# Kernel optimization log

Hardware: AMD Instinct MI355X
Metric: run time of the kernel (lower is better)

Reference implementation:

```python
import jax, jax.numpy as jnp
import numpy as np

B, T, V, H, L = 2048, 128, 256, 20, 15  # batch, seq_len, vocab, hidden, max_label


def setup_inputs() -> dict:
    key = jax.random.key(0)
    ks = jax.random.split(key, 8)
    g = lambda k, shape, s: (jax.random.normal(k, shape, jnp.float32) * s)
    return {
        "x": jax.random.randint(ks[0], (B, T), 0, V, dtype=jnp.int32),
        "W0": g(ks[1], (V, 3 * H), 0.06),   # input kernel layer 0 [V, 3H] (z|r|h)
        "U0": g(ks[2], (H, 3 * H), 0.2),    # recurrent kernel layer 0
        "b0i": jnp.zeros((3 * H,), jnp.float32),  # input bias (reset_after=True split bias)
        "b0r": jnp.zeros((3 * H,), jnp.float32),  # recurrent bias
        "W1": g(ks[3], (H, 3 * H), 0.2),
        "U1": g(ks[4], (H, 3 * H), 0.2),
        "b1i": jnp.zeros((3 * H,), jnp.float32),
        "b1r": jnp.zeros((3 * H,), jnp.float32),
        "Wd": g(ks[5], (H, L), 0.2),
        "bd": jnp.zeros((L,), jnp.float32),
        "drop_rate": 0,  # identity dropout (deterministic reference)
    }


def _gru_cell(h, xw, U, br):
    # Keras GRUCell with reset_after=True:
    #   xw = x @ W + b_in  (precomputed), rec = h @ U + b_rec
    rec = h @ U + br
    xz, xr, xh = jnp.split(xw, 3, axis=-1)
    rz, rr, rh = jnp.split(rec, 3, axis=-1)
    z = jax.nn.sigmoid(xz + rz)
    r = jax.nn.sigmoid(xr + rr)
    hh = jnp.tanh(xh + r * rh)
    return z * h + (1.0 - z) * hh


def reference(x, W0, U0, b0i, b0r, W1, U1, b1i, b1r, Wd, bd, drop_rate):
    # one_hot(x) @ W0 == gather rows of W0 (same math, no [B,T,V] materialization)
    xW0 = W0[x] + b0i                 # [B, T, 3H]
    xW0 = jnp.swapaxes(xW0, 0, 1)     # [T, B, 3H] for scan over time

    def step(carry, xw_t):
        h0, h1 = carry
        h0 = _gru_cell(h0, xw_t, U0, b0r)
        xw1 = h0 @ W1 + b1i
        h1 = _gru_cell(h1, xw1, U1, b1r)
        return (h0, h1), None

    h0 = jnp.zeros((x.shape[0], H), W0.dtype)
    h1 = jnp.zeros((x.shape[0], H), W0.dtype)
    (h0, h1), _ = jax.lax.scan(step, (h0, h1), xW0)
    # tf.nn.dropout with rate 0 is the identity
    out = h1
    logits = jax.nn.softmax(out @ Wd + bd, axis=-1)  # [B, L]
    return logits
```

## Files before the change

kernel.cpp:

```cpp
#include <hip/hip_runtime.h>


#define BB 2048
#define TT 128
#define HH 20
#define LL 15
#define H3 60

typedef float v2f __attribute__((ext_vector_type(2)));

__device__ __forceinline__ float bclane(float v, int k) {
    return __int_as_float(__builtin_amdgcn_readlane(__float_as_int(v), k));
}
__device__ __forceinline__ float dpp_rshr1(float v) {
    return __int_as_float(__builtin_amdgcn_update_dpp(
        0, __float_as_int(v), 0x111, 0xF, 0xF, true));
}
__device__ __forceinline__ float fast_rcp(float x) { return __builtin_amdgcn_rcpf(x); }
__device__ __forceinline__ float sigm(float x) { return fast_rcp(1.f + __expf(-x)); }
__device__ __forceinline__ float tanh_f(float x) { return 1.f - 2.f * fast_rcp(1.f + __expf(2.f * x)); }
#define PIN(v) asm volatile("" : "+v"(v))
#define LDSFENCE() asm volatile("" ::: "memory")

extern "C" __global__ __launch_bounds__(256)
__attribute__((amdgpu_waves_per_eu(2, 2)))
void gru2_kernel(const int* __restrict__ x, const float* __restrict__ W0,
                 const float* __restrict__ U0, const float* __restrict__ b0i,
                 const float* __restrict__ b0r, const float* __restrict__ W1,
                 const float* __restrict__ U1, const float* __restrict__ b1i,
                 const float* __restrict__ b1r, const float* __restrict__ Wd,
                 const float* __restrict__ bd, float* __restrict__ out)
{
    if (((blockIdx.x >> 3) ^ (blockIdx.x >> 8)) & 1)
        __builtin_amdgcn_s_sleep(6);

    const int lane = threadIdx.x & 63;
    const int w = threadIdx.x >> 6;
    const int b = blockIdx.x * 4 + w;
    const int row = lane >> 4;
    const int pos = lane & 15;
    const int pc  = (pos < 15) ? pos : 14;
    const int u   = pc / 3;
    const int p3  = pc % 3;
    const int j   = row * 5 + u;
    const bool home = (pos < 15) && (p3 == 2);
    const int col = p3 * 20 + j;

    __shared__ __align__(16) float hbuf[4][2][24];
    float* h0buf = &hbuf[w][0][0];
    float* h1buf = &hbuf[w][1][0];
    const float4* h0q = (const float4*)h0buf;
    const float4* h1q = (const float4*)h1buf;
    if (home) { h0buf[j] = 0.f; h1buf[j] = 0.f; }
    LDSFENCE();

    v2f u0p[10], w1p[10], u1p[10];
#pragma unroll
    for (int q = 0; q < 10; ++q) {
        const int k0 = (2 * q) * H3, k1 = (2 * q + 1) * H3;
        u0p[q] = v2f{U0[k0 + col], U0[k1 + col]};
        w1p[q] = v2f{W1[k0 + col], W1[k1 + col]};
        u1p[q] = v2f{U1[k0 + col], U1[k1 + col]};
    }
#pragma unroll
    for (int q = 0; q < 10; ++q) { PIN(u0p[q]); PIN(w1p[q]); PIN(u1p[q]); }
    float bi0 = b0i[col], br0 = b0r[col], bi1 = b1i[col], br1 = b1r[col];
    PIN(bi0); PIN(br0); PIN(bi1); PIN(br1);

    const int* xrow = x + b * TT;
    const int tokA = xrow[lane];
    const int tokB = xrow[64 + lane];

    float h0 = 0.f, h1 = 0.f;

    const int tok0 = __builtin_amdgcn_readlane(tokA, 0);
    const int tok1 = __builtin_amdgcn_readlane(tokA, 1);
    int tokn2 = __builtin_amdgcn_readlane(tokA, 2);
    float xw_cur = W0[tok0 * H3 + col] + bi0;
    float xw_nxt = W0[tok1 * H3 + col];

    float4 c0[5], c1[5];
    float rec0, xw1, rec1;

#define DOTS()                                                                \
    {                                                                         \
        v2f a0a = v2f{br0, 0.f}, a0b = v2f{0.f, 0.f};                         \
        v2f a1a = v2f{bi1, 0.f}, a1b = v2f{0.f, 0.f};                         \
        v2f a2a = v2f{br1, 0.f}, a2b = v2f{0.f, 0.f};                         \
        _Pragma("unroll")                                                     \
        for (int q = 0; q < 5; ++q) {                                         \
            const v2f hA = v2f{c0[q].x, c0[q].y}, hB = v2f{c0[q].z, c0[q].w}; \
            a0a = __builtin_elementwise_fma(hA, u0p[2 * q], a0a);             \
            a0b = __builtin_elementwise_fma(hB, u0p[2 * q + 1], a0b);         \
            a1a = __builtin_elementwise_fma(hA, w1p[2 * q], a1a);             \
            a1b = __builtin_elementwise_fma(hB, w1p[2 * q + 1], a1b);         \
        }                                                                     \
        _Pragma("unroll")                                                     \
        for (int q = 0; q < 5; ++q) {                                         \
            const v2f gA = v2f{c1[q].x, c1[q].y}, gB = v2f{c1[q].z, c1[q].w}; \
            a2a = __builtin_elementwise_fma(gA, u1p[2 * q], a2a);             \
            a2b = __builtin_elementwise_fma(gB, u1p[2 * q + 1], a2b);         \
        }                                                                     \
        { const v2f t = a0a + a0b; rec0 = t.x + t.y; }                        \
        { const v2f t = a1a + a1b; xw1  = t.x + t.y; }                        \
        { const v2f t = a2a + a2b; rec1 = t.x + t.y; }                        \
    }

    {
        const float pf = W0[tokn2 * H3 + col];
        const int tokn3 = __builtin_amdgcn_readlane(tokA, 3);
        const float sg0 = sigm(xw_cur + br0);
        const float rv0 = dpp_rshr1(sg0);
        const float zv0 = dpp_rshr1(rv0);
        const float hh0 = tanh_f(xw_cur + rv0 * br0);
        h0 = fmaf(zv0, h0 - hh0, hh0);
        if (home) h0buf[j] = h0;
        LDSFENCE();
#pragma unroll
        for (int q = 0; q < 5; ++q) { c0[q] = h0q[q]; c1[q] = h1q[q]; }
        xw_cur = xw_nxt + bi0; xw_nxt = pf; tokn2 = tokn3;
        DOTS();
    }

#pragma unroll 2
    for (int i = 1; i < TT; ++i) {
        const int t3 = (i + 3 < TT) ? (i + 3) : (TT - 1);
        const float pf = W0[tokn2 * H3 + col];
        const int tokn3 = __builtin_amdgcn_readlane(t3 < 64 ? tokA : tokB, t3 & 63);

        const float sg0 = sigm(xw_cur + rec0);
        const float rv0 = dpp_rshr1(sg0);
        const float zv0 = dpp_rshr1(rv0);
        const float hh0 = tanh_f(xw_cur + rv0 * rec0);
        h0 = fmaf(zv0, h0 - hh0, hh0);
        if (home) h0buf[j] = h0;
        LDSFENCE();
#pragma unroll
        for (int q = 0; q < 5; ++q) c0[q] = h0q[q];

        const float sg1 = sigm(xw1 + rec1);
        const float rv1 = dpp_rshr1(sg1);
        const float zv1 = dpp_rshr1(rv1);
        const float hh1 = tanh_f(xw1 + rv1 * rec1);
        h1 = fmaf(zv1, h1 - hh1, hh1);
        if (home) h1buf[j] = h1;
        LDSFENCE();
#pragma unroll
        for (int q = 0; q < 5; ++q) c1[q] = h1q[q];

        xw_cur = xw_nxt + bi0; xw_nxt = pf; tokn2 = tokn3;

        DOTS();
    }

    {
        const float sg1 = sigm(xw1 + rec1);
        const float rv1 = dpp_rshr1(sg1);
        const float zv1 = dpp_rshr1(rv1);
        const float hh1 = tanh_f(xw1 + rv1 * rec1);
        h1 = fmaf(zv1, h1 - hh1, hh1);
        if (home) h1buf[j] = h1;
        LDSFENCE();
    }

    const int l = lane < LL ? lane : LL - 1;
    float acc = bd[l];
#pragma unroll
    for (int k = 0; k < HH; ++k)
        acc = fmaf(h1buf[k], Wd[k * LL + l], acc);

    float m = acc;
#pragma unroll
    for (int i = 0; i < LL; ++i) m = fmaxf(m, bclane(acc, i));
    const float e = __expf(acc - m);
    float s = 0.f;
#pragma unroll
    for (int i = 0; i < LL; ++i) s += bclane(e, i);
    const float pr = e * fast_rcp(s);

    if (lane < LL) out[b * LL + lane] = pr;
}

extern "C" void kernel_launch(void* const* d_in, const int* in_sizes, int n_in,
                              void* d_out, int out_size, void* d_ws, size_t ws_size,
                              hipStream_t stream) {
    const int*   x   = (const int*)  d_in[0];
    const float* W0  = (const float*)d_in[1];
    const float* U0  = (const float*)d_in[2];
    const float* b0i = (const float*)d_in[3];
    const float* b0r = (const float*)d_in[4];
    const float* W1  = (const float*)d_in[5];
    const float* U1  = (const float*)d_in[6];
    const float* b1i = (const float*)d_in[7];
    const float* b1r = (const float*)d_in[8];
    const float* Wd  = (const float*)d_in[9];
    const float* bd  = (const float*)d_in[10];
    float* out = (float*)d_out;

    dim3 grid(BB / 4), block(256);
    hipLaunchKernelGGL(gru2_kernel, grid, block, 0, stream,
                       x, W0, U0, b0i, b0r, W1, U1, b1i, b1r, Wd, bd, out);
}
```

Baseline: 124.1 us.

## Broadcast hidden state via readlane instead of LDS round-trip

Replaces the per-step LDS store/load of h0 and h1 with v_readlane broadcasts from the lanes that own each hidden unit, feeding scalar FMAs instead of packed v2f FMAs. It also drops the staggered s_sleep at kernel start and preloads the dense-layer weights into registers. The aim is to cut LDS latency and wait counts out of the serial recurrence. In exchange it adds 40 readlanes per step, which are SALU/VALU-serialized and may cost more than the LDS path, and it gives up the packed FMA throughput.

```diff
diff --git a/kernel.cpp b/kernel.cpp
--- a/kernel.cpp
+++ b/kernel.cpp
@@ -7,10 +7,12 @@
 #define LL 15
 #define H3 60
 
-typedef float v2f __attribute__((ext_vector_type(2)));
-
 __device__ __forceinline__ float bclane(float v, int k) {
     return __int_as_float(__builtin_amdgcn_readlane(__float_as_int(v), k));
+}
+__device__ __forceinline__ float rdhome(float v, int j) {
+    const int ln = ((j / 5) << 4) + (j % 5) * 3 + 2;
+    return __int_as_float(__builtin_amdgcn_readlane(__float_as_int(v), ln));
 }
 __device__ __forceinline__ float dpp_rshr1(float v) {
     return __int_as_float(__builtin_amdgcn_update_dpp(
@@ -20,7 +22,6 @@
 __device__ __forceinline__ float sigm(float x) { return fast_rcp(1.f + __expf(-x)); }
 __device__ __forceinline__ float tanh_f(float x) { return 1.f - 2.f * fast_rcp(1.f + __expf(2.f * x)); }
 #define PIN(v) asm volatile("" : "+v"(v))
-#define LDSFENCE() asm volatile("" ::: "memory")
 
 extern "C" __global__ __launch_bounds__(256)
 __attribute__((amdgpu_waves_per_eu(2, 2)))
@@ -31,9 +32,6 @@
                  const float* __restrict__ b1r, const float* __restrict__ Wd,
                  const float* __restrict__ bd, float* __restrict__ out)
 {
-    if (((blockIdx.x >> 3) ^ (blockIdx.x >> 8)) & 1)
-        __builtin_amdgcn_s_sleep(6);
-
     const int lane = threadIdx.x & 63;
     const int w = threadIdx.x >> 6;
     const int b = blockIdx.x * 4 + w;
@@ -42,30 +40,28 @@
     const int pc  = (pos < 15) ? pos : 14;
     const int u   = pc / 3;
     const int p3  = pc % 3;
-    const int j   = row * 5 + u;
-    const bool home = (pos < 15) && (p3 == 2);
-    const int col = p3 * 20 + j;
+    const int col = p3 * 20 + (row * 5 + u);
 
-    __shared__ __align__(16) float hbuf[4][2][24];
-    float* h0buf = &hbuf[w][0][0];
-    float* h1buf = &hbuf[w][1][0];
-    const float4* h0q = (const float4*)h0buf;
-    const float4* h1q = (const float4*)h1buf;
-    if (home) { h0buf[j] = 0.f; h1buf[j] = 0.f; }
-    LDSFENCE();
-
-    v2f u0p[10], w1p[10], u1p[10];
+    float u0c[HH], w1c[HH], u1c[HH];
 #pragma unroll
-    for (int q = 0; q < 10; ++q) {
-        const int k0 = (2 * q) * H3, k1 = (2 * q + 1) * H3;
-        u0p[q] = v2f{U0[k0 + col], U0[k1 + col]};
-        w1p[q] = v2f{W1[k0 + col], W1[k1 + col]};
-        u1p[q] = v2f{U1[k0 + col], U1[k1 + col]};
+    for (int k = 0; k < HH; ++k) {
+        u0c[k] = U0[k * H3 + col];
+        w1c[k] = W1[k * H3 + col];
+        u1c[k] = U1[k * H3 + col];
     }
 #pragma unroll
-    for (int q = 0; q < 10; ++q) { PIN(u0p[q]); PIN(w1p[q]); PIN(u1p[q]); }
+    for (int k = 0; k < HH; ++k) { PIN(u0c[k]); PIN(w1c[k]); PIN(u1c[k]); }
     float bi0 = b0i[col], br0 = b0r[col], bi1 = b1i[col], br1 = b1r[col];
     PIN(bi0); PIN(br0); PIN(bi1); PIN(br1);
+
+    const int l = lane < LL ? lane : LL - 1;
+    float wdc[HH];
+#pragma unroll
+    for (int k = 0; k < HH; ++k) wdc[k] = Wd[k * LL + l];
+    float bdl = bd[l];
+#pragma unroll
+    for (int k = 0; k < HH; ++k) PIN(wdc[k]);
+    PIN(bdl);
 
     const int* xrow = x + b * TT;
     const int tokA = xrow[lane];
@@ -79,31 +75,29 @@
     float xw_cur = W0[tok0 * H3 + col] + bi0;
     float xw_nxt = W0[tok1 * H3 + col];
 
-    float4 c0[5], c1[5];
+    float s0[HH];
     float rec0, xw1, rec1;
 
 #define DOTS()                                                                \
     {                                                                         \
-        v2f a0a = v2f{br0, 0.f}, a0b = v2f{0.f, 0.f};                         \
-        v2f a1a = v2f{bi1, 0.f}, a1b = v2f{0.f, 0.f};                         \
-        v2f a2a = v2f{br1, 0.f}, a2b = v2f{0.f, 0.f};                         \
+        float a0 = br0, e0 = 0.f;                                             \
+        float a1 = bi1, e1 = 0.f;                                             \
+        float a2 = br1, e2 = 0.f;                                             \
         _Pragma("unroll")                                                     \
-        for (int q = 0; q < 5; ++q) {                                         \
-            const v2f hA = v2f{c0[q].x, c0[q].y}, hB = v2f{c0[q].z, c0[q].w}; \
-            a0a = __builtin_elementwise_fma(hA, u0p[2 * q], a0a);             \
-            a0b = __builtin_elementwise_fma(hB, u0p[2 * q + 1], a0b);         \
-            a1a = __builtin_elementwise_fma(hA, w1p[2 * q], a1a);             \
-            a1b = __builtin_elementwise_fma(hB, w1p[2 * q + 1], a1b);         \
+        for (int k = 0; k < HH / 2; ++k) {                                    \
+            a0 = fmaf(s0[2 * k],     u0c[2 * k],     a0);                     \
+            e0 = fmaf(s0[2 * k + 1], u0c[2 * k + 1], e0);                     \
+            a1 = fmaf(s0[2 * k],     w1c[2 * k],     a1);                     \
+            e1 = fmaf(s0[2 * k + 1], w1c[2 * k + 1], e1);                     \
         }                                                                     \
         _Pragma("unroll")                                                     \
-        for (int q = 0; q < 5; ++q) {                                         \
-            const v2f gA = v2f{c1[q].x, c1[q].y}, gB = v2f{c1[q].z, c1[q].w}; \
-            a2a = __builtin_elementwise_fma(gA, u1p[2 * q], a2a);             \
-            a2b = __builtin_elementwise_fma(gB, u1p[2 * q + 1], a2b);         \
+        for (int k = 0; k < HH / 2; ++k) {                                    \
+            const float g0 = rdhome(h1, 2 * k);                               \
+            const float g1 = rdhome(h1, 2 * k + 1);                           \
+            a2 = fmaf(g0, u1c[2 * k],     a2);                                \
+            e2 = fmaf(g1, u1c[2 * k + 1], e2);                                \
         }                                                                     \
-        { const v2f t = a0a + a0b; rec0 = t.x + t.y; }                        \
-        { const v2f t = a1a + a1b; xw1  = t.x + t.y; }                        \
-        { const v2f t = a2a + a2b; rec1 = t.x + t.y; }                        \
+        rec0 = a0 + e0; xw1 = a1 + e1; rec1 = a2 + e2;                        \
     }
 
     {
@@ -114,10 +108,8 @@
         const float zv0 = dpp_rshr1(rv0);
         const float hh0 = tanh_f(xw_cur + rv0 * br0);
         h0 = fmaf(zv0, h0 - hh0, hh0);
-        if (home) h0buf[j] = h0;
-        LDSFENCE();
 #pragma unroll
-        for (int q = 0; q < 5; ++q) { c0[q] = h0q[q]; c1[q] = h1q[q]; }
+        for (int k = 0; k < HH; ++k) s0[k] = rdhome(h0, k);
         xw_cur = xw_nxt + bi0; xw_nxt = pf; tokn2 = tokn3;
         DOTS();
     }
@@ -133,41 +125,35 @@
         const float zv0 = dpp_rshr1(rv0);
         const float hh0 = tanh_f(xw_cur + rv0 * rec0);
         h0 = fmaf(zv0, h0 - hh0, hh0);
-        if (home) h0buf[j] = h0;
-        LDSFENCE();
 #pragma unroll
-        for (int q = 0; q < 5; ++q) c0[q] = h0q[q];
+        for (int k = 0; k < HH; ++k) s0[k] = rdhome(h0, k);
 
         const float sg1 = sigm(xw1 + rec1);
         const float rv1 = dpp_rshr1(sg1);
         const float zv1 = dpp_rshr1(rv1);
         const float hh1 = tanh_f(xw1 + rv1 * rec1);
         h1 = fmaf(zv1, h1 - hh1, hh1);
-        if (home) h1buf[j] = h1;
-        LDSFENCE();
-#pragma unroll
-        for (int q = 0; q < 5; ++q) c1[q] = h1q[q];
 
         xw_cur = xw_nxt + bi0; xw_nxt = pf; tokn2 = tokn3;
 
         DOTS();
     }
 
+    float s1h[HH];
     {
         const float sg1 = sigm(xw1 + rec1);
         const float rv1 = dpp_rshr1(sg1);
         const float zv1 = dpp_rshr1(rv1);
         const float hh1 = tanh_f(xw1 + rv1 * rec1);
         h1 = fmaf(zv1, h1 - hh1, hh1);
-        if (home) h1buf[j] = h1;
-        LDSFENCE();
+#pragma unroll
+        for (int k = 0; k < HH; ++k) s1h[k] = rdhome(h1, k);
     }
 
-    const int l = lane < LL ? lane : LL - 1;
-    float acc = bd[l];
+    float acc = bdl;
 #pragma unroll
     for (int k = 0; k < HH; ++k)
-        acc = fmaf(h1buf[k], Wd[k * LL + l], acc);
+        acc = fmaf(s1h[k], wdc[k], acc);
 
     float m = acc;
 #pragma unroll
```

Measured after the change: 142.5 us. 1.15x slower.

## Fold gate prescale into weights, use exp2 gates, and reorder layer-1 dot

Applied to the files above, without the earlier changes.

Pre-multiplies the weights and biases by -log2(e), or by -2·log2(e) for the candidate gate, so each gate needs only a raw exp2 with no extra multiply. Sigmoid and tanh share one GATES macro, and the z gate is read with a single shift-by-2 DPP instead of two chained shift-by-1 moves. The layer-1 recurrent dot product is split out and now runs just before the layer-1 gate, so it uses last step's h1 and no longer waits for the new h0. The staggered s_sleep at block start is also removed. The risk is a small change in floating-point rounding from the prescaled weights.

```diff
diff --git a/kernel.cpp b/kernel.cpp
--- a/kernel.cpp
+++ b/kernel.cpp
@@ -9,6 +9,12 @@
 
 typedef float v2f __attribute__((ext_vector_type(2)));
 
+#if __has_builtin(__builtin_amdgcn_exp2f)
+#define EXP2(x) __builtin_amdgcn_exp2f(x)
+#else
+#define EXP2(x) exp2f(x)
+#endif
+
 __device__ __forceinline__ float bclane(float v, int k) {
     return __int_as_float(__builtin_amdgcn_readlane(__float_as_int(v), k));
 }
@@ -16,9 +22,11 @@
     return __int_as_float(__builtin_amdgcn_update_dpp(
         0, __float_as_int(v), 0x111, 0xF, 0xF, true));
 }
+__device__ __forceinline__ float dpp_rshr2(float v) {
+    return __int_as_float(__builtin_amdgcn_update_dpp(
+        0, __float_as_int(v), 0x112, 0xF, 0xF, true));
+}
 __device__ __forceinline__ float fast_rcp(float x) { return __builtin_amdgcn_rcpf(x); }
-__device__ __forceinline__ float sigm(float x) { return fast_rcp(1.f + __expf(-x)); }
-__device__ __forceinline__ float tanh_f(float x) { return 1.f - 2.f * fast_rcp(1.f + __expf(2.f * x)); }
 #define PIN(v) asm volatile("" : "+v"(v))
 #define LDSFENCE() asm volatile("" ::: "memory")
 
@@ -31,9 +39,6 @@
                  const float* __restrict__ b1r, const float* __restrict__ Wd,
                  const float* __restrict__ bd, float* __restrict__ out)
 {
-    if (((blockIdx.x >> 3) ^ (blockIdx.x >> 8)) & 1)
-        __builtin_amdgcn_s_sleep(6);
-
     const int lane = threadIdx.x & 63;
     const int w = threadIdx.x >> 6;
     const int b = blockIdx.x * 4 + w;
@@ -46,6 +51,8 @@
     const bool home = (pos < 15) && (p3 == 2);
     const int col = p3 * 20 + j;
 
+    const float gsc = (p3 == 2) ? -2.8853900817779268f : -1.4426950408889634f;
+
     __shared__ __align__(16) float hbuf[4][2][24];
     float* h0buf = &hbuf[w][0][0];
     float* h1buf = &hbuf[w][1][0];
@@ -58,13 +65,14 @@
 #pragma unroll
     for (int q = 0; q < 10; ++q) {
         const int k0 = (2 * q) * H3, k1 = (2 * q + 1) * H3;
-        u0p[q] = v2f{U0[k0 + col], U0[k1 + col]};
-        w1p[q] = v2f{W1[k0 + col], W1[k1 + col]};
-        u1p[q] = v2f{U1[k0 + col], U1[k1 + col]};
+        u0p[q] = v2f{U0[k0 + col] * gsc, U0[k1 + col] * gsc};
+        w1p[q] = v2f{W1[k0 + col] * gsc, W1[k1 + col] * gsc};
+        u1p[q] = v2f{U1[k0 + col] * gsc, U1[k1 + col] * gsc};
     }
 #pragma unroll
     for (int q = 0; q < 10; ++q) { PIN(u0p[q]); PIN(w1p[q]); PIN(u1p[q]); }
-    float bi0 = b0i[col], br0 = b0r[col], bi1 = b1i[col], br1 = b1r[col];
+    float bi0 = b0i[col] * gsc, br0 = b0r[col] * gsc;
+    float bi1 = b1i[col] * gsc, br1 = b1r[col] * gsc;
     PIN(bi0); PIN(br0); PIN(bi1); PIN(br1);
 
     const int* xrow = x + b * TT;
@@ -76,17 +84,16 @@
     const int tok0 = __builtin_amdgcn_readlane(tokA, 0);
     const int tok1 = __builtin_amdgcn_readlane(tokA, 1);
     int tokn2 = __builtin_amdgcn_readlane(tokA, 2);
-    float xw_cur = W0[tok0 * H3 + col] + bi0;
+    float xw_cur = fmaf(W0[tok0 * H3 + col], gsc, bi0);
     float xw_nxt = W0[tok1 * H3 + col];
 
     float4 c0[5], c1[5];
     float rec0, xw1, rec1;
 
-#define DOTS()                                                                \
+#define DOT01()                                                               \
     {                                                                         \
         v2f a0a = v2f{br0, 0.f}, a0b = v2f{0.f, 0.f};                         \
         v2f a1a = v2f{bi1, 0.f}, a1b = v2f{0.f, 0.f};                         \
-        v2f a2a = v2f{br1, 0.f}, a2b = v2f{0.f, 0.f};                         \
         _Pragma("unroll")                                                     \
         for (int q = 0; q < 5; ++q) {                                         \
             const v2f hA = v2f{c0[q].x, c0[q].y}, hB = v2f{c0[q].z, c0[q].w}; \
@@ -95,31 +102,42 @@
             a1a = __builtin_elementwise_fma(hA, w1p[2 * q], a1a);             \
             a1b = __builtin_elementwise_fma(hB, w1p[2 * q + 1], a1b);         \
         }                                                                     \
+        { const v2f t = a0a + a0b; rec0 = t.x + t.y; }                        \
+        { const v2f t = a1a + a1b; xw1  = t.x + t.y; }                        \
+    }
+#define DOT2()                                                                \
+    {                                                                         \
+        v2f a2a = v2f{br1, 0.f}, a2b = v2f{0.f, 0.f};                         \
         _Pragma("unroll")                                                     \
         for (int q = 0; q < 5; ++q) {                                         \
             const v2f gA = v2f{c1[q].x, c1[q].y}, gB = v2f{c1[q].z, c1[q].w}; \
             a2a = __builtin_elementwise_fma(gA, u1p[2 * q], a2a);             \
             a2b = __builtin_elementwise_fma(gB, u1p[2 * q + 1], a2b);         \
         }                                                                     \
-        { const v2f t = a0a + a0b; rec0 = t.x + t.y; }                        \
-        { const v2f t = a1a + a1b; xw1  = t.x + t.y; }                        \
         { const v2f t = a2a + a2b; rec1 = t.x + t.y; }                        \
+    }
+#define GATES(XW, REC, H)                                                     \
+    {                                                                         \
+        const float e  = EXP2((XW) + (REC));                                  \
+        const float t  = fast_rcp(1.f + e);                                   \
+        const float rv = dpp_rshr1(t);                                        \
+        const float zv = dpp_rshr2(t);                                        \
+        const float eh = EXP2(fmaf(rv, (REC), (XW)));                         \
+        const float th = fast_rcp(1.f + eh);                                  \
+        const float hh = fmaf(2.f, th, -1.f);                                 \
+        H = fmaf(zv, (H) - hh, hh);                                           \
     }
 
     {
         const float pf = W0[tokn2 * H3 + col];
         const int tokn3 = __builtin_amdgcn_readlane(tokA, 3);
-        const float sg0 = sigm(xw_cur + br0);
-        const float rv0 = dpp_rshr1(sg0);
-        const float zv0 = dpp_rshr1(rv0);
-        const float hh0 = tanh_f(xw_cur + rv0 * br0);
-        h0 = fmaf(zv0, h0 - hh0, hh0);
+        GATES(xw_cur, br0, h0);
         if (home) h0buf[j] = h0;
         LDSFENCE();
 #pragma unroll
         for (int q = 0; q < 5; ++q) { c0[q] = h0q[q]; c1[q] = h1q[q]; }
-        xw_cur = xw_nxt + bi0; xw_nxt = pf; tokn2 = tokn3;
-        DOTS();
+        xw_cur = fmaf(xw_nxt, gsc, bi0); xw_nxt = pf; tokn2 = tokn3;
+        DOT01();
     }
 
 #pragma unroll 2
@@ -128,37 +146,28 @@
         const float pf = W0[tokn2 * H3 + col];
         const int tokn3 = __builtin_amdgcn_readlane(t3 < 64 ? tokA : tokB, t3 & 63);
 
-        const float sg0 = sigm(xw_cur + rec0);
-        const float rv0 = dpp_rshr1(sg0);
-        const float zv0 = dpp_rshr1(rv0);
-        const float hh0 = tanh_f(xw_cur + rv0 * rec0);
-        h0 = fmaf(zv0, h0 - hh0, hh0);
+        GATES(xw_cur, rec0, h0);
         if (home) h0buf[j] = h0;
         LDSFENCE();
 #pragma unroll
         for (int q = 0; q < 5; ++q) c0[q] = h0q[q];
 
-        const float sg1 = sigm(xw1 + rec1);
-        const float rv1 = dpp_rshr1(sg1);
-        const float zv1 = dpp_rshr1(rv1);
-        const float hh1 = tanh_f(xw1 + rv1 * rec1);
-        h1 = fmaf(zv1, h1 - hh1, hh1);
+        DOT2();
+
+        GATES(xw1, rec1, h1);
         if (home) h1buf[j] = h1;
         LDSFENCE();
 #pragma unroll
         for (int q = 0; q < 5; ++q) c1[q] = h1q[q];
 
-        xw_cur = xw_nxt + bi0; xw_nxt = pf; tokn2 = tokn3;
-
-        DOTS();
+        xw_cur = fmaf(xw_nxt, gsc, bi0); xw_nxt = pf; tokn2 = tokn3;
+
+        DOT01();
     }
 
     {
-        const float sg1 = sigm(xw1 + rec1);
-        const float rv1 = dpp_rshr1(sg1);
-        const float zv1 = dpp_rshr1(rv1);
-        const float hh1 = tanh_f(xw1 + rv1 * rec1);
-        h1 = fmaf(zv1, h1 - hh1, hh1);
+        DOT2();
+        GATES(xw1, rec1, h1);
         if (home) h1buf[j] = h1;
         LDSFENCE();
     }
```

Measured after the change: 121.2 us. -2.3%, faster.
